# Kernel optimization log

Hardware: AMD Instinct MI355X
Metric: run time of the kernel (lower is better)

Reference implementation:

```python
import jax, jax.numpy as jnp
import numpy as np

N_RES = 768
C = 128  # act_dim == num_intermediate_channel
EPS = 1e-5


def _layer_norm(x, w, b):
    mu = jnp.mean(x, axis=-1, keepdims=True)
    var = jnp.mean(jnp.square(x - mu), axis=-1, keepdims=True)
    return (x - mu) * jax.lax.rsqrt(var + EPS) * w + b


def _linear(x, w, b):
    # torch Linear: w is [out, in]
    return jnp.einsum('ijc,dc->ijd', x, w) + b


def setup_inputs() -> dict:
    key = jax.random.key(0)
    ks = jax.random.split(key, 16)
    s = 1.0 / np.sqrt(C)
    d = {
        'act': jax.random.normal(ks[0], (N_RES, N_RES, C), jnp.float32),
        'mask': jnp.ones((N_RES, N_RES), jnp.float32),
        'ln_in_w': jnp.ones((C,), jnp.float32),
        'ln_in_b': jnp.zeros((C,), jnp.float32),
        'lp_w': jax.random.normal(ks[1], (C, C), jnp.float32) * s,
        'lp_b': jnp.zeros((C,), jnp.float32),
        'rp_w': jax.random.normal(ks[2], (C, C), jnp.float32) * s,
        'rp_b': jnp.zeros((C,), jnp.float32),
        'lg_w': jax.random.normal(ks[3], (C, C), jnp.float32) * s,
        'lg_b': jnp.ones((C,), jnp.float32),
        'rg_w': jax.random.normal(ks[4], (C, C), jnp.float32) * s,
        'rg_b': jnp.ones((C,), jnp.float32),
        'cln_w': jnp.ones((C,), jnp.float32),
        'cln_b': jnp.zeros((C,), jnp.float32),
        'op_w': jax.random.normal(ks[5], (C, C), jnp.float32) * s,
        'op_b': jnp.zeros((C,), jnp.float32),
        'gl_w': jax.random.normal(ks[6], (C, C), jnp.float32) * s,
        'gl_b': jnp.ones((C,), jnp.float32),
    }
    return d


def reference(act, mask, ln_in_w, ln_in_b, lp_w, lp_b, rp_w, rp_b,
              lg_w, lg_b, rg_w, rg_b, cln_w, cln_b, op_w, op_b, gl_w, gl_b):
    m = mask[..., None]                                   # [N, N, 1]
    act_ln = _layer_norm(act, ln_in_w, ln_in_b)           # [N, N, C]
    left = m * _linear(act_ln, lp_w, lp_b) * jax.nn.sigmoid(_linear(act_ln, lg_w, lg_b))
    right = m * _linear(act_ln, rp_w, rp_b) * jax.nn.sigmoid(_linear(act_ln, rg_w, rg_b))
    # outgoing-edges triangle multiplication
    out = jnp.einsum('ikc,jkc->ijc', left, right)          # [N, N, C]
    out = _layer_norm(out, cln_w, cln_b)
    out = _linear(out, op_w, op_b)
    gate = jax.nn.sigmoid(_linear(act_ln, gl_w, gl_b))
    return out * gate
```

## Files before the change

### kernel.cpp

```cpp
#include <hip/hip_runtime.h>
#include <math.h>


#define NRES 768
#define CD 128
#define NN (768 * 768)

typedef unsigned short u16;
typedef unsigned int u32;
typedef __attribute__((ext_vector_type(8))) short bf16x8;
typedef __attribute__((ext_vector_type(4))) float f32x4;

__device__ __forceinline__ float b2f(u16 u) {
  union { u32 i; float f; } v; v.i = ((u32)u) << 16; return v.f;
}
__device__ __forceinline__ u16 f2bf(float f) {
  union { float f; u32 i; } v; v.f = f;
  return (u16)((v.i + 0x7fffu + ((v.i >> 16) & 1u)) >> 16);
}
__device__ __forceinline__ float sigm(float x) { return 1.0f / (1.0f + __expf(-x)); }

__device__ __forceinline__ void async16(u16* lds, const u16* g) {
  __builtin_amdgcn_global_load_lds((const __attribute__((address_space(1))) void*)g,
                                   (__attribute__((address_space(3))) void*)lds, 16, 0, 0);
}

__global__ void k_convw(const float* __restrict__ a, const float* __restrict__ b,
                        const float* __restrict__ c, const float* __restrict__ d,
                        const float* __restrict__ e, const float* __restrict__ f,
                        u16* __restrict__ wb) {
  int i = blockIdx.x * 256 + threadIdx.x;
  int m = i >> 14, r = i & 16383;
  const float* s = (m == 0) ? a : (m == 1) ? b : (m == 2) ? c : (m == 3) ? d : (m == 4) ? e : f;
  wb[i] = f2bf(s[r]);
}

__global__ __launch_bounds__(256) void k_proj(
    const float* __restrict__ act, const float* __restrict__ mask,
    const float* __restrict__ lnw, const float* __restrict__ lnb,
    const u16* __restrict__ wb,
    const float* __restrict__ lpb, const float* __restrict__ lgb,
    const float* __restrict__ rpb, const float* __restrict__ rgb,
    const float* __restrict__ glb,
    u16* __restrict__ left_t, u16* __restrict__ right_t, u16* __restrict__ gate) {
  __shared__ u16 sx[128][128];
  __shared__ u16 st[128 * 72];
  __shared__ float fmask[128];
  const int t = threadIdx.x;
  const int pos0 = blockIdx.x * 128;
  const int l = t & 63, w = t >> 6;
  const int lr = l & 15, g4 = l >> 4;

  {
    const int r = t >> 1, q = t & 1;
    const float* arow = act + (size_t)(pos0 + r) * CD + q * 64;
    float4 xv[16];
    float s = 0.f, ss = 0.f;
#pragma unroll
    for (int j = 0; j < 16; ++j) {
      xv[j] = *(const float4*)(arow + j * 4);
      s += xv[j].x + xv[j].y + xv[j].z + xv[j].w;
      ss += xv[j].x * xv[j].x + xv[j].y * xv[j].y + xv[j].z * xv[j].z + xv[j].w * xv[j].w;
    }
    s += __shfl_xor(s, 1); ss += __shfl_xor(ss, 1);
    float mu = s * (1.0f / CD);
    float rs = rsqrtf(ss * (1.0f / CD) - mu * mu + 1e-5f);
    const int key = (r & 7) << 3;
#pragma unroll
    for (int j = 0; j < 16; j += 2) {
      u16 o[8] __attribute__((aligned(16)));
      const float* xx = (const float*)&xv[j];
      int c0 = q * 64 + j * 4;
#pragma unroll
      for (int e2 = 0; e2 < 8; ++e2)
        o[e2] = f2bf((xx[e2] - mu) * rs * lnw[c0 + e2] + lnb[c0 + e2]);
      *(bf16x8*)&sx[r][c0 ^ key] = *(const bf16x8*)o;
    }
    if (t < 128) fmask[t] = mask[pos0 + t];
  }
  __syncthreads();

  auto pair_pass = [&](const u16* __restrict__ WP, const u16* __restrict__ WG,
                       const float* __restrict__ bP, const float* __restrict__ bG,
                       u16* __restrict__ dst) {
    bf16x8 bp[2][4], bg[2][4];
    float biasP[2], biasG[2];
    int dd[2];
#pragma unroll
    for (int c2 = 0; c2 < 2; ++c2) {
      dd[c2] = w * 32 + c2 * 16 + lr;
#pragma unroll
      for (int kk = 0; kk < 4; ++kk) {
        bp[c2][kk] = *(const bf16x8*)&WP[dd[c2] * CD + kk * 32 + g4 * 8];
        bg[c2][kk] = *(const bf16x8*)&WG[dd[c2] * CD + kk * 32 + g4 * 8];
      }
      biasP[c2] = bP[dd[c2]];
      biasG[c2] = bG[dd[c2]];
    }
#pragma unroll
    for (int mc = 0; mc < 2; ++mc) {
#pragma unroll
      for (int m = 0; m < 4; ++m) {
        const int row = mc * 64 + m * 16 + lr;
        const int key = (row & 7) << 3;
        bf16x8 af[4];
#pragma unroll
        for (int kk = 0; kk < 4; ++kk)
          af[kk] = *(const bf16x8*)&sx[row][(kk * 32 + g4 * 8) ^ key];
#pragma unroll
        for (int c2 = 0; c2 < 2; ++c2) {
          f32x4 aP = {0.f, 0.f, 0.f, 0.f}, aG = {0.f, 0.f, 0.f, 0.f};
#pragma unroll
          for (int kk = 0; kk < 4; ++kk) {
            aP = __builtin_amdgcn_mfma_f32_16x16x32_bf16(af[kk], bp[c2][kk], aP, 0, 0, 0);
            aG = __builtin_amdgcn_mfma_f32_16x16x32_bf16(af[kk], bg[c2][kk], aG, 0, 0, 0);
          }
          const int rowc = m * 16 + g4 * 4;
          u16 o[4] __attribute__((aligned(8)));
#pragma unroll
          for (int r = 0; r < 4; ++r)
            o[r] = f2bf((aP[r] + biasP[c2]) * sigm(aG[r] + biasG[c2]) * fmask[mc * 64 + rowc + r]);
          *(uint2*)&st[dd[c2] * 72 + rowc] = *(const uint2*)o;
        }
      }
      __syncthreads();
#pragma unroll
      for (int p = 0; p < 4; ++p) {
        const int d = p * 32 + (t >> 3), off = (t & 7) * 8;
        *(bf16x8*)&dst[(size_t)d * NN + pos0 + mc * 64 + off] = *(const bf16x8*)&st[d * 72 + off];
      }
      __syncthreads();
    }
  };

  pair_pass(wb, wb + 16384, lpb, lgb, left_t);
  pair_pass(wb + 2 * 16384, wb + 3 * 16384, rpb, rgb, right_t);

  {
    const u16* WG = wb + 4 * 16384;
    bf16x8 bg[2][4];
    float biasG[2];
    int dd[2];
#pragma unroll
    for (int c2 = 0; c2 < 2; ++c2) {
      dd[c2] = w * 32 + c2 * 16 + lr;
#pragma unroll
      for (int kk = 0; kk < 4; ++kk)
        bg[c2][kk] = *(const bf16x8*)&WG[dd[c2] * CD + kk * 32 + g4 * 8];
      biasG[c2] = glb[dd[c2]];
    }
#pragma unroll
    for (int mc = 0; mc < 2; ++mc) {
#pragma unroll
      for (int m = 0; m < 4; ++m) {
        const int row = mc * 64 + m * 16 + lr;
        const int key = (row & 7) << 3;
        bf16x8 af[4];
#pragma unroll
        for (int kk = 0; kk < 4; ++kk)
          af[kk] = *(const bf16x8*)&sx[row][(kk * 32 + g4 * 8) ^ key];
#pragma unroll
        for (int c2 = 0; c2 < 2; ++c2) {
          f32x4 aG = {0.f, 0.f, 0.f, 0.f};
#pragma unroll
          for (int kk = 0; kk < 4; ++kk)
            aG = __builtin_amdgcn_mfma_f32_16x16x32_bf16(af[kk], bg[c2][kk], aG, 0, 0, 0);
          const int rowc = m * 16 + g4 * 4;
#pragma unroll
          for (int r = 0; r < 4; ++r)
            st[(rowc + r) * 136 + dd[c2]] = f2bf(sigm(aG[r] + biasG[c2]));
        }
      }
      __syncthreads();
      {
        const int row = t >> 2, dc = (t & 3) * 32;
#pragma unroll
        for (int jj = 0; jj < 4; ++jj)
          *(bf16x8*)&gate[(size_t)(pos0 + mc * 64 + row) * CD + dc + jj * 8] =
              *(const bf16x8*)&st[row * 136 + dc + jj * 8];
      }
      __syncthreads();
    }
  }
}

__global__ __launch_bounds__(256) void k_tri(
    const u16* __restrict__ left_t, const u16* __restrict__ right_t,
    u16* __restrict__ out_t) {
  __shared__ u16 sA[128 * 32];
  __shared__ u16 sB[128 * 32];
  const int t = threadIdx.x, l = t & 63, w = t >> 6;
  const int bid = blockIdx.x;
  const int xcd = bid & 7, idx = bid >> 3;
  const int c = xcd * 16 + idx / 36;
  const int tile = idx - (idx / 36) * 36;
  const int ti = tile / 6, tj = tile - (tile / 6) * 6;
  const u16* A = left_t + (size_t)c * NN + (size_t)ti * 128 * NRES;
  const u16* B = right_t + (size_t)c * NN + (size_t)tj * 128 * NRES;
  const int lr = l & 15, lk = (l >> 4) * 8;
  const int wr = (w >> 1) * 64, wc = (w & 1) * 64;
  f32x4 acc[4][4];
#pragma unroll
  for (int m = 0; m < 4; ++m)
#pragma unroll
    for (int n = 0; n < 4; ++n) acc[m][n] = (f32x4){0.f, 0.f, 0.f, 0.f};

  const int wbase = t & ~63;
  for (int ks = 0; ks < 24; ++ks) {
    const int k0 = ks * 32;
#pragma unroll
    for (int it = 0; it < 2; ++it) {
      int li = it * 256 + t;
      async16(&sA[(it * 256 + wbase) * 8], A + (size_t)(li >> 2) * NRES + k0 + (li & 3) * 8);
      async16(&sB[(it * 256 + wbase) * 8], B + (size_t)(li >> 2) * NRES + k0 + (li & 3) * 8);
    }
    __syncthreads();
    bf16x8 av[4], bv[4];
#pragma unroll
    for (int m = 0; m < 4; ++m) av[m] = *(const bf16x8*)&sA[(wr + m * 16 + lr) * 32 + lk];
#pragma unroll
    for (int n = 0; n < 4; ++n) bv[n] = *(const bf16x8*)&sB[(wc + n * 16 + lr) * 32 + lk];
#pragma unroll
    for (int m = 0; m < 4; ++m)
#pragma unroll
      for (int n = 0; n < 4; ++n)
        acc[m][n] = __builtin_amdgcn_mfma_f32_16x16x32_bf16(av[m], bv[n], acc[m][n], 0, 0, 0);
    __syncthreads();
  }

  u16* O = out_t + (size_t)c * NN;
  const int r0l = (l >> 4) << 2;
#pragma unroll
  for (int m = 0; m < 4; ++m) {
#pragma unroll
    for (int n = 0; n < 4; ++n) {
      int row = ti * 128 + wr + m * 16 + r0l;
      int col = tj * 128 + wc + n * 16 + lr;
#pragma unroll
      for (int r = 0; r < 4; ++r)
        O[(size_t)(row + r) * NRES + col] = f2bf(acc[m][n][r]);
    }
  }
}

__global__ __launch_bounds__(128) void k_post(
    const u16* __restrict__ out_t, const u16* __restrict__ gate,
    const float* __restrict__ clnw, const float* __restrict__ clnb,
    const u16* __restrict__ wop, const float* __restrict__ opb,
    float* __restrict__ out) {
  __shared__ u16 sx[128][136];
  __shared__ float smu[128], srs[128];
  __shared__ float swv[128], sbv[128];
  const int t = threadIdx.x;
  const int pos0 = blockIdx.x * 128;

  swv[t] = clnw[t];
  sbv[t] = clnb[t];

  {
    const size_t p = (size_t)pos0 + t;
    float s = 0.f, ss = 0.f;
    const int key = ((t >> 3) & 7) << 4;
#pragma unroll
    for (int ch = 0; ch < 16; ++ch) {
      u16 u[8] __attribute__((aligned(16)));
#pragma unroll
      for (int e = 0; e < 8; ++e) u[e] = out_t[(size_t)(ch * 8 + e) * NN + p];
#pragma unroll
      for (int e = 0; e < 8; ++e) { float f = b2f(u[e]); s += f; ss += f * f; }
      *(bf16x8*)&sx[t][(ch * 8) ^ key] = *(const bf16x8*)u;
    }
    float mu = s * (1.0f / CD);
    smu[t] = mu;
    srs[t] = rsqrtf(ss * (1.0f / CD) - mu * mu + 1e-5f);
  }
  __syncthreads();

  const int l = t & 63, w = t >> 6;
  const int lr = l & 15, lk8 = (l >> 4) * 8;
  bf16x8 af[4][4];
#pragma unroll
  for (int m = 0; m < 4; ++m) {
    const int pr = w * 64 + m * 16 + lr;
    const float mu = smu[pr], rs = srs[pr];
    const int key = ((pr >> 3) & 7) << 4;
#pragma unroll
    for (int kk = 0; kk < 4; ++kk) {
      const int c0 = kk * 32 + lk8;
      bf16x8 raw = *(const bf16x8*)&sx[pr][c0 ^ key];
      u16 o[8] __attribute__((aligned(16)));
#pragma unroll
      for (int e = 0; e < 8; ++e)
        o[e] = f2bf((b2f((u16)raw[e]) - mu) * rs * swv[c0 + e] + sbv[c0 + e]);
      af[m][kk] = *(const bf16x8*)o;
    }
  }
  const int r0l = (l >> 4) << 2;
#pragma unroll
  for (int ct = 0; ct < 8; ++ct) {
    const int d = ct * 16 + lr;
    bf16x8 bv[4];
#pragma unroll
    for (int kk = 0; kk < 4; ++kk)
      bv[kk] = *(const bf16x8*)&wop[d * CD + kk * 32 + lk8];
    const float bo = opb[d];
#pragma unroll
    for (int m = 0; m < 4; ++m) {
      f32x4 acc = {0.f, 0.f, 0.f, 0.f};
#pragma unroll
      for (int kk = 0; kk < 4; ++kk)
        acc = __builtin_amdgcn_mfma_f32_16x16x32_bf16(af[m][kk], bv[kk], acc, 0, 0, 0);
      const int prow = w * 64 + m * 16 + r0l;
#pragma unroll
      for (int r = 0; r < 4; ++r) {
        size_t pp = (size_t)(pos0 + prow + r) * CD + d;
        out[pp] = (acc[r] + bo) * b2f(gate[pp]);
      }
    }
  }
}

extern "C" void kernel_launch(void* const* d_in, const int* in_sizes, int n_in,
                              void* d_out, int out_size, void* d_ws, size_t ws_size,
                              hipStream_t stream) {
  (void)in_sizes; (void)n_in; (void)out_size; (void)ws_size;
  const float* act  = (const float*)d_in[0];
  const float* mask = (const float*)d_in[1];
  const float* lnw  = (const float*)d_in[2];
  const float* lnb  = (const float*)d_in[3];
  const float* lpw  = (const float*)d_in[4];
  const float* lpb  = (const float*)d_in[5];
  const float* rpw  = (const float*)d_in[6];
  const float* rpb  = (const float*)d_in[7];
  const float* lgw  = (const float*)d_in[8];
  const float* lgb  = (const float*)d_in[9];
  const float* rgw  = (const float*)d_in[10];
  const float* rgb  = (const float*)d_in[11];
  const float* clnw = (const float*)d_in[12];
  const float* clnb = (const float*)d_in[13];
  const float* opw  = (const float*)d_in[14];
  const float* opb  = (const float*)d_in[15];
  const float* glw  = (const float*)d_in[16];
  const float* glb  = (const float*)d_in[17];

  char* wsb = (char*)d_ws;
  u16* wb = (u16*)wsb;
  const size_t SZ = (size_t)NN * CD * 2;
  size_t off = (size_t)1 << 20;
  u16* left_t  = (u16*)(wsb + off); off += SZ;
  u16* right_t = (u16*)(wsb + off); off += SZ;
  u16* gate    = (u16*)(wsb + off); off += SZ;
  u16* out_t   = (u16*)(wsb + off); off += SZ;

  k_convw<<<384, 256, 0, stream>>>(lpw, lgw, rpw, rgw, glw, opw, wb);
  k_proj<<<NN / 128, 256, 0, stream>>>(act, mask, lnw, lnb, wb,
                                       lpb, lgb, rpb, rgb, glb,
                                       left_t, right_t, gate);
  k_tri<<<4608, 256, 0, stream>>>(left_t, right_t, out_t);
  k_post<<<NN / 128, 128, 0, stream>>>(out_t, gate, clnw, clnb,
                                       wb + 5 * 16384, opb, (float*)d_out);
}
```

Before: 826.8 us.

## Double-buffer tri-matmul LDS, drop proj LDS staging, widen post kernel, faster sigmoid

The triangle-multiplication kernel now uses two LDS buffers, so the async loads for the next k-slice are issued before the current slice is consumed. The projection kernel drops its LDS transpose staging and the barriers around it, and writes left/right/gate values straight to global memory. The post kernel now runs 256 threads, with two threads per row sharing the LayerNorm reduction through a shuffle. Sigmoid uses the hardware exp2/rcp intrinsics, float-to-bf16 uses the HIP conversion, and occupancy hints are added to the launch bounds. The direct global stores in the projection kernel are narrow and scattered, which risks poor write coalescing, especially the 2-byte gate stores.

```diff
diff --git a/kernel.cpp b/kernel.cpp
--- a/kernel.cpp
+++ b/kernel.cpp
@@ -1,4 +1,5 @@
 #include <hip/hip_runtime.h>
+#include <hip/hip_bf16.h>
 #include <math.h>
 
 
@@ -15,10 +16,12 @@
   union { u32 i; float f; } v; v.i = ((u32)u) << 16; return v.f;
 }
 __device__ __forceinline__ u16 f2bf(float f) {
-  union { float f; u32 i; } v; v.f = f;
-  return (u16)((v.i + 0x7fffu + ((v.i >> 16) & 1u)) >> 16);
-}
-__device__ __forceinline__ float sigm(float x) { return 1.0f / (1.0f + __expf(-x)); }
+  __hip_bfloat16 h = __float2bfloat16(f);
+  return *reinterpret_cast<u16*>(&h);
+}
+__device__ __forceinline__ float sigm(float x) {
+  return __builtin_amdgcn_rcpf(1.0f + __builtin_amdgcn_exp2f(x * -1.44269504f));
+}
 
 __device__ __forceinline__ void async16(u16* lds, const u16* g) {
   __builtin_amdgcn_global_load_lds((const __attribute__((address_space(1))) void*)g,
@@ -35,7 +38,7 @@
   wb[i] = f2bf(s[r]);
 }
 
-__global__ __launch_bounds__(256) void k_proj(
+__global__ __launch_bounds__(256, 4) void k_proj(
     const float* __restrict__ act, const float* __restrict__ mask,
     const float* __restrict__ lnw, const float* __restrict__ lnb,
     const u16* __restrict__ wb,
@@ -44,7 +47,6 @@
     const float* __restrict__ glb,
     u16* __restrict__ left_t, u16* __restrict__ right_t, u16* __restrict__ gate) {
   __shared__ u16 sx[128][128];
-  __shared__ u16 st[128 * 72];
   __shared__ float fmask[128];
   const int t = threadIdx.x;
   const int pos0 = blockIdx.x * 128;
@@ -107,6 +109,10 @@
 #pragma unroll
         for (int kk = 0; kk < 4; ++kk)
           af[kk] = *(const bf16x8*)&sx[row][(kk * 32 + g4 * 8) ^ key];
+        const int rowc = m * 16 + g4 * 4;
+        float fm[4];
+#pragma unroll
+        for (int r = 0; r < 4; ++r) fm[r] = fmask[mc * 64 + rowc + r];
 #pragma unroll
         for (int c2 = 0; c2 < 2; ++c2) {
           f32x4 aP = {0.f, 0.f, 0.f, 0.f}, aG = {0.f, 0.f, 0.f, 0.f};
@@ -115,21 +121,13 @@
             aP = __builtin_amdgcn_mfma_f32_16x16x32_bf16(af[kk], bp[c2][kk], aP, 0, 0, 0);
             aG = __builtin_amdgcn_mfma_f32_16x16x32_bf16(af[kk], bg[c2][kk], aG, 0, 0, 0);
           }
-          const int rowc = m * 16 + g4 * 4;
           u16 o[4] __attribute__((aligned(8)));
 #pragma unroll
           for (int r = 0; r < 4; ++r)
-            o[r] = f2bf((aP[r] + biasP[c2]) * sigm(aG[r] + biasG[c2]) * fmask[mc * 64 + rowc + r]);
-          *(uint2*)&st[dd[c2] * 72 + rowc] = *(const uint2*)o;
+            o[r] = f2bf((aP[r] + biasP[c2]) * sigm(aG[r] + biasG[c2]) * fm[r]);
+          *(uint2*)&dst[(size_t)dd[c2] * NN + pos0 + mc * 64 + rowc] = *(const uint2*)o;
         }
       }
-      __syncthreads();
-#pragma unroll
-      for (int p = 0; p < 4; ++p) {
-        const int d = p * 32 + (t >> 3), off = (t & 7) * 8;
-        *(bf16x8*)&dst[(size_t)d * NN + pos0 + mc * 64 + off] = *(const bf16x8*)&st[d * 72 + off];
-      }
-      __syncthreads();
     }
   };
 
@@ -159,36 +157,27 @@
 #pragma unroll
         for (int kk = 0; kk < 4; ++kk)
           af[kk] = *(const bf16x8*)&sx[row][(kk * 32 + g4 * 8) ^ key];
+        const int posb = pos0 + mc * 64 + m * 16 + g4 * 4;
 #pragma unroll
         for (int c2 = 0; c2 < 2; ++c2) {
           f32x4 aG = {0.f, 0.f, 0.f, 0.f};
 #pragma unroll
           for (int kk = 0; kk < 4; ++kk)
             aG = __builtin_amdgcn_mfma_f32_16x16x32_bf16(af[kk], bg[c2][kk], aG, 0, 0, 0);
-          const int rowc = m * 16 + g4 * 4;
 #pragma unroll
           for (int r = 0; r < 4; ++r)
-            st[(rowc + r) * 136 + dd[c2]] = f2bf(sigm(aG[r] + biasG[c2]));
+            gate[(size_t)(posb + r) * CD + dd[c2]] = f2bf(sigm(aG[r] + biasG[c2]));
         }
       }
-      __syncthreads();
-      {
-        const int row = t >> 2, dc = (t & 3) * 32;
-#pragma unroll
-        for (int jj = 0; jj < 4; ++jj)
-          *(bf16x8*)&gate[(size_t)(pos0 + mc * 64 + row) * CD + dc + jj * 8] =
-              *(const bf16x8*)&st[row * 136 + dc + jj * 8];
-      }
-      __syncthreads();
-    }
-  }
-}
-
-__global__ __launch_bounds__(256) void k_tri(
+    }
+  }
+}
+
+__global__ __launch_bounds__(256, 4) void k_tri(
     const u16* __restrict__ left_t, const u16* __restrict__ right_t,
     u16* __restrict__ out_t) {
-  __shared__ u16 sA[128 * 32];
-  __shared__ u16 sB[128 * 32];
+  __shared__ u16 sA[2][128 * 32];
+  __shared__ u16 sB[2][128 * 32];
   const int t = threadIdx.x, l = t & 63, w = t >> 6;
   const int bid = blockIdx.x;
   const int xcd = bid & 7, idx = bid >> 3;
@@ -199,27 +188,32 @@
   const u16* B = right_t + (size_t)c * NN + (size_t)tj * 128 * NRES;
   const int lr = l & 15, lk = (l >> 4) * 8;
   const int wr = (w >> 1) * 64, wc = (w & 1) * 64;
+  const int wbase = t & ~63;
   f32x4 acc[4][4];
 #pragma unroll
   for (int m = 0; m < 4; ++m)
 #pragma unroll
     for (int n = 0; n < 4; ++n) acc[m][n] = (f32x4){0.f, 0.f, 0.f, 0.f};
 
-  const int wbase = t & ~63;
-  for (int ks = 0; ks < 24; ++ks) {
-    const int k0 = ks * 32;
+  auto stage = [&](int p, int k0) {
 #pragma unroll
     for (int it = 0; it < 2; ++it) {
       int li = it * 256 + t;
-      async16(&sA[(it * 256 + wbase) * 8], A + (size_t)(li >> 2) * NRES + k0 + (li & 3) * 8);
-      async16(&sB[(it * 256 + wbase) * 8], B + (size_t)(li >> 2) * NRES + k0 + (li & 3) * 8);
-    }
-    __syncthreads();
+      async16(&sA[p][(it * 256 + wbase) * 8], A + (size_t)(li >> 2) * NRES + k0 + (li & 3) * 8);
+      async16(&sB[p][(it * 256 + wbase) * 8], B + (size_t)(li >> 2) * NRES + k0 + (li & 3) * 8);
+    }
+  };
+
+  stage(0, 0);
+  __syncthreads();
+  for (int ks = 0; ks < 24; ++ks) {
+    const int p = ks & 1;
+    if (ks < 23) stage(p ^ 1, (ks + 1) * 32);
     bf16x8 av[4], bv[4];
 #pragma unroll
-    for (int m = 0; m < 4; ++m) av[m] = *(const bf16x8*)&sA[(wr + m * 16 + lr) * 32 + lk];
-#pragma unroll
-    for (int n = 0; n < 4; ++n) bv[n] = *(const bf16x8*)&sB[(wc + n * 16 + lr) * 32 + lk];
+    for (int m = 0; m < 4; ++m) av[m] = *(const bf16x8*)&sA[p][(wr + m * 16 + lr) * 32 + lk];
+#pragma unroll
+    for (int n = 0; n < 4; ++n) bv[n] = *(const bf16x8*)&sB[p][(wc + n * 16 + lr) * 32 + lk];
 #pragma unroll
     for (int m = 0; m < 4; ++m)
 #pragma unroll
@@ -243,7 +237,7 @@
   }
 }
 
-__global__ __launch_bounds__(128) void k_post(
+__global__ __launch_bounds__(256, 4) void k_post(
     const u16* __restrict__ out_t, const u16* __restrict__ gate,
     const float* __restrict__ clnw, const float* __restrict__ clnb,
     const u16* __restrict__ wop, const float* __restrict__ opb,
@@ -254,34 +248,36 @@
   const int t = threadIdx.x;
   const int pos0 = blockIdx.x * 128;
 
-  swv[t] = clnw[t];
-  sbv[t] = clnb[t];
+  if (t < 128) { swv[t] = clnw[t]; sbv[t] = clnb[t]; }
 
   {
-    const size_t p = (size_t)pos0 + t;
+    const int r = t >> 1, q = t & 1;
+    const size_t p = (size_t)pos0 + r;
     float s = 0.f, ss = 0.f;
-    const int key = ((t >> 3) & 7) << 4;
-#pragma unroll
-    for (int ch = 0; ch < 16; ++ch) {
+    const int key = ((r >> 3) & 7) << 4;
+#pragma unroll
+    for (int ch = 0; ch < 8; ++ch) {
+      const int c0 = q * 64 + ch * 8;
       u16 u[8] __attribute__((aligned(16)));
 #pragma unroll
-      for (int e = 0; e < 8; ++e) u[e] = out_t[(size_t)(ch * 8 + e) * NN + p];
+      for (int e = 0; e < 8; ++e) u[e] = out_t[(size_t)(c0 + e) * NN + p];
 #pragma unroll
       for (int e = 0; e < 8; ++e) { float f = b2f(u[e]); s += f; ss += f * f; }
-      *(bf16x8*)&sx[t][(ch * 8) ^ key] = *(const bf16x8*)u;
-    }
+      *(bf16x8*)&sx[r][c0 ^ key] = *(const bf16x8*)u;
+    }
+    s += __shfl_xor(s, 1); ss += __shfl_xor(ss, 1);
     float mu = s * (1.0f / CD);
-    smu[t] = mu;
-    srs[t] = rsqrtf(ss * (1.0f / CD) - mu * mu + 1e-5f);
+    float rs = rsqrtf(ss * (1.0f / CD) - mu * mu + 1e-5f);
+    if (q == 0) { smu[r] = mu; srs[r] = rs; }
   }
   __syncthreads();
 
   const int l = t & 63, w = t >> 6;
   const int lr = l & 15, lk8 = (l >> 4) * 8;
-  bf16x8 af[4][4];
-#pragma unroll
-  for (int m = 0; m < 4; ++m) {
-    const int pr = w * 64 + m * 16 + lr;
+  bf16x8 af[2][4];
+#pragma unroll
+  for (int m = 0; m < 2; ++m) {
+    const int pr = w * 32 + m * 16 + lr;
     const float mu = smu[pr], rs = srs[pr];
     const int key = ((pr >> 3) & 7) << 4;
 #pragma unroll
@@ -305,12 +301,12 @@
       bv[kk] = *(const bf16x8*)&wop[d * CD + kk * 32 + lk8];
     const float bo = opb[d];
 #pragma unroll
-    for (int m = 0; m < 4; ++m) {
+    for (int m = 0; m < 2; ++m) {
       f32x4 acc = {0.f, 0.f, 0.f, 0.f};
 #pragma unroll
       for (int kk = 0; kk < 4; ++kk)
         acc = __builtin_amdgcn_mfma_f32_16x16x32_bf16(af[m][kk], bv[kk], acc, 0, 0, 0);
-      const int prow = w * 64 + m * 16 + r0l;
+      const int prow = w * 32 + m * 16 + r0l;
 #pragma unroll
       for (int r = 0; r < 4; ++r) {
         size_t pp = (size_t)(pos0 + prow + r) * CD + d;
@@ -357,6 +353,6 @@
                                        lpb, lgb, rpb, rgb, glb,
                                        left_t, right_t, gate);
   k_tri<<<4608, 256, 0, stream>>>(left_t, right_t, out_t);
-  k_post<<<NN / 128, 128, 0, stream>>>(out_t, gate, clnw, clnb,
+  k_post<<<NN / 128, 256, 0, stream>>>(out_t, gate, clnw, clnb,
                                        wb + 5 * 16384, opb, (float*)d_out);
 }
```

Result: slower. 977.0 us (+18.2%).
